# Kernel optimization log

Hardware: AMD Instinct MI355X
Metric: run time of the kernel (lower is better)

## Reference

```python
import jax, jax.numpy as jnp
import numpy as np

D = 3  # input dim, hardcoded in source


def _jet_linear(c0, c1, c2, W, b):
    # Taylor-mode (raw-derivative coefficients) through y = x @ W^T + b.
    # Bias only affects the 0th coefficient; higher coefficients are linear.
    y0 = jnp.einsum('bdi,oi->bdo', c0, W) + b
    y1 = jnp.einsum('bdi,oi->bdo', c1, W)
    y2 = jnp.einsum('bdi,oi->bdo', c2, W)
    return y0, y1, y2


def _jet_tanh(c0, c1, c2):
    # g(t) with g(0)=c0, g'(0)=c1, g''(0)=c2; f = tanh(g):
    #   f(0)  = tanh(c0)
    #   f'(0) = sech^2(c0) * c1
    #   f''(0)= sech^2(c0) * c2 - 2 tanh(c0) sech^2(c0) * c1^2
    y0 = jnp.tanh(c0)
    s = 1.0 - y0 * y0  # sech^2
    y1 = s * c1
    y2 = s * c2 - 2.0 * y0 * s * (c1 * c1)
    return y0, y1, y2


def setup_inputs() -> dict:
    key = jax.random.key(0)
    ks = jax.random.split(key, 7)
    B = 131072
    x = jax.random.normal(ks[0], (B, D), dtype=jnp.float32)
    # Kaiming-ish small init so tanh does not saturate
    W1 = jax.random.normal(ks[1], (128, D), dtype=jnp.float32) * (1.0 / np.sqrt(D))
    b1 = jax.random.normal(ks[2], (128,), dtype=jnp.float32) * 0.01
    W2 = jax.random.normal(ks[3], (64, 128), dtype=jnp.float32) * (1.0 / np.sqrt(128))
    b2 = jax.random.normal(ks[4], (64,), dtype=jnp.float32) * 0.01
    W3 = jax.random.normal(ks[5], (1, 64), dtype=jnp.float32) * (1.0 / np.sqrt(64))
    b3 = jax.random.normal(ks[6], (1,), dtype=jnp.float32) * 0.01
    return {'x': x, 'W1': W1, 'b1': b1, 'W2': W2, 'b2': b2, 'W3': W3, 'b3': b3}


def reference(x, W1, b1, W2, b2, W3, b3):
    # x: [B, D]. Propagate a k=2 jet along each of the D coordinate
    # directions (vmapped over the direction axis d), then sum the 2nd
    # coefficients -> Laplacian. Returns [B, 1].
    B = x.shape[0]
    dt = x.dtype
    X0 = jnp.broadcast_to(x[:, None, :], (B, D, D))            # replicate(x, D)
    X1 = jnp.broadcast_to(jnp.eye(D, dtype=dt), (B, D, D))     # eye(D)
    X2 = jnp.zeros((B, D, D), dtype=dt)                         # zeros(D, D)
    c = _jet_linear(X0, X1, X2, W1, b1)
    c = _jet_tanh(*c)
    c = _jet_linear(*c, W2, b2)
    c = _jet_tanh(*c)
    F0, F1, F2 = _jet_linear(*c, W3, b3)                        # F2: [B, D, 1]
    return F2.sum(axis=1)                                       # sum_vmapped -> [B, 1]
```

## Files before the change

### kernel.cpp

```cpp
#include <hip/hip_runtime.h>


typedef _Float16 h2 __attribute__((ext_vector_type(2)));
typedef _Float16 h4 __attribute__((ext_vector_type(4)));
typedef _Float16 h8 __attribute__((ext_vector_type(8)));
typedef float f32x4 __attribute__((ext_vector_type(4)));

#define BLOCK 256
constexpr int DH1 = 128;
constexpr int DH2 = 64;

constexpr size_t WS_APACK = 0;
constexpr size_t WS_W1P   = 16384;
constexpr size_t WS_WQ2   = 18432;

__device__ __forceinline__ float fast_tanh(float x) {
    float e = __builtin_amdgcn_exp2f(x * 2.885390081777926814f);
    return fmaf(-2.0f, __builtin_amdgcn_rcpf(e + 1.0f), 1.0f);
}

__device__ __forceinline__ h2 pk(float a, float b) {
    auto r = __builtin_amdgcn_cvt_pkrtz(a, b);
    return __builtin_bit_cast(h2, r);
}

__device__ __forceinline__ h8 cat4(h2 a, h2 b, h2 c, h2 d) {
    h4 lo = __builtin_shufflevector(a, b, 0, 1, 2, 3);
    h4 hi = __builtin_shufflevector(c, d, 0, 1, 2, 3);
    return __builtin_shufflevector(lo, hi, 0, 1, 2, 3, 4, 5, 6, 7);
}

__global__ void pack_kernel(const float* __restrict__ W1, const float* __restrict__ b1,
                            const float* __restrict__ W2,
                            _Float16* __restrict__ apack,
                            float4* __restrict__ w1p, float* __restrict__ wq2)
{
    const int t = threadIdx.x, bid = blockIdx.x;
    #pragma unroll
    for (int u = 0; u < 4; ++u) {
        const int e  = bid * 1024 + u * 256 + t;
        const int i  = e & 7;
        const int l  = (e >> 3) & 63;
        const int m  = (e >> 9) & 3;
        const int kk = (e >> 11) & 3;
        const int k  = m * 16 + (l & 15);
        const int j  = kk * 32 + (l >> 4) * 8 + i;
        apack[e] = (_Float16)W2[k * DH1 + j];
    }
    if (bid == 0 && t < DH1) {
        const float wx = W1[t*3+0], wy = W1[t*3+1], wz = W1[t*3+2];
        w1p[t] = make_float4(wx, wy, wz, b1[t]);
        wq2[t] = -2.0f * (wx*wx + wy*wy + wz*wz);
    }
}

__global__ __launch_bounds__(BLOCK, 3) void lap_main(
        const float* __restrict__ x,
        const h8* __restrict__ apack,
        const float4* __restrict__ w1p, const float* __restrict__ wq2,
        const float* __restrict__ b2, const float* __restrict__ w3,
        float* __restrict__ out, int B)
{
    const int t    = threadIdx.x;
    const int lane = t & 63;
    const int wave = t >> 6;
    const int bcol = lane & 15;
    const int g    = lane >> 4;
    const int braw = blockIdx.x * 64 + wave * 16 + bcol;
    const int b    = (braw < B) ? braw : (B - 1);

    const float x0 = x[b*3+0];
    const float x1 = x[b*3+1];
    const float x2 = x[b*3+2];

    f32x4 acc[5][4];
    #pragma unroll
    for (int f = 0; f < 5; ++f)
        #pragma unroll
        for (int m = 0; m < 4; ++m)
            acc[f][m] = (f32x4){0.f, 0.f, 0.f, 0.f};

    #pragma unroll
    for (int kk = 0; kk < 4; ++kk) {
        h8 fa[4];
        #pragma unroll
        for (int m = 0; m < 4; ++m)
            fa[m] = apack[(kk*4 + m) * 64 + lane];

        h2 P0[4], P1[4], P2[4], P3[4], P4[4];
        #pragma unroll
        for (int ii = 0; ii < 4; ++ii) {
            const int j0 = kk*32 + g*8 + ii*2;
            const float4 wa = w1p[j0];
            const float4 wb = w1p[j0 + 1];
            const float  qa = wq2[j0];
            const float  qb = wq2[j0 + 1];

            const float prea = fmaf(x0, wa.x, fmaf(x1, wa.y, fmaf(x2, wa.z, wa.w)));
            const float ea   = __builtin_amdgcn_exp2f(prea * 2.885390081777926814f);
            const float ra   = __builtin_amdgcn_rcpf(ea + 1.0f);
            const float ha   = fmaf(-2.0f, ra, 1.0f);
            const float sa   = fmaf(-ha, ha, 1.0f);

            const float preb = fmaf(x0, wb.x, fmaf(x1, wb.y, fmaf(x2, wb.z, wb.w)));
            const float eb   = __builtin_amdgcn_exp2f(preb * 2.885390081777926814f);
            const float rb   = __builtin_amdgcn_rcpf(eb + 1.0f);
            const float hb   = fmaf(-2.0f, rb, 1.0f);
            const float sb   = fmaf(-hb, hb, 1.0f);

            P0[ii] = pk(ha,          hb);
            P1[ii] = pk(sa * wa.x,   sb * wb.x);
            P2[ii] = pk(sa * wa.y,   sb * wb.y);
            P3[ii] = pk(sa * wa.z,   sb * wb.z);
            P4[ii] = pk((ha*sa)*qa,  (hb*sb)*qb);
        }
        const h8 F0 = cat4(P0[0], P0[1], P0[2], P0[3]);
        const h8 F1 = cat4(P1[0], P1[1], P1[2], P1[3]);
        const h8 F2 = cat4(P2[0], P2[1], P2[2], P2[3]);
        const h8 F3 = cat4(P3[0], P3[1], P3[2], P3[3]);
        const h8 F4 = cat4(P4[0], P4[1], P4[2], P4[3]);

        #pragma unroll
        for (int m = 0; m < 4; ++m) {
            acc[0][m] = __builtin_amdgcn_mfma_f32_16x16x32_f16(fa[m], F0, acc[0][m], 0, 0, 0);
            acc[1][m] = __builtin_amdgcn_mfma_f32_16x16x32_f16(fa[m], F1, acc[1][m], 0, 0, 0);
            acc[2][m] = __builtin_amdgcn_mfma_f32_16x16x32_f16(fa[m], F2, acc[2][m], 0, 0, 0);
            acc[3][m] = __builtin_amdgcn_mfma_f32_16x16x32_f16(fa[m], F3, acc[3][m], 0, 0, 0);
            acc[4][m] = __builtin_amdgcn_mfma_f32_16x16x32_f16(fa[m], F4, acc[4][m], 0, 0, 0);
        }
    }

    float partial = 0.0f;
    #pragma unroll
    for (int m = 0; m < 4; ++m) {
        const int kb = m*16 + g*4;
        const f32x4 b2v = *reinterpret_cast<const f32x4*>(b2 + kb);
        const f32x4 w3v = *reinterpret_cast<const f32x4*>(w3 + kb);
        #pragma unroll
        for (int r = 0; r < 4; ++r) {
            const float z0 = acc[0][m][r] + b2v[r];
            const float g0 = fast_tanh(z0);
            const float s2 = fmaf(-g0, g0, 1.0f);
            const float qd = acc[1][m][r]*acc[1][m][r]
                           + acc[2][m][r]*acc[2][m][r]
                           + acc[3][m][r]*acc[3][m][r];
            const float G2 = s2 * fmaf(-2.0f * g0, qd, acc[4][m][r]);
            partial = fmaf(w3v[r], G2, partial);
        }
    }

    partial += __shfl_xor(partial, 16);
    partial += __shfl_xor(partial, 32);

    if (g == 0 && braw < B) out[braw] = partial;
}

extern "C" void kernel_launch(void* const* d_in, const int* in_sizes, int n_in,
                              void* d_out, int out_size, void* d_ws, size_t ws_size,
                              hipStream_t stream) {
    const float* x  = (const float*)d_in[0];
    const float* W1 = (const float*)d_in[1];
    const float* b1 = (const float*)d_in[2];
    const float* W2 = (const float*)d_in[3];
    const float* b2 = (const float*)d_in[4];
    const float* W3 = (const float*)d_in[5];
    float* out = (float*)d_out;

    char* ws = (char*)d_ws;
    _Float16* apack = (_Float16*)(ws + WS_APACK);
    float4*   w1p   = (float4*)  (ws + WS_W1P);
    float*    wq2   = (float*)   (ws + WS_WQ2);

    const int B = in_sizes[0] / 3;

    pack_kernel<<<8, BLOCK, 0, stream>>>(W1, b1, W2, apack, w1p, wq2);

    const int grid = (B + 63) / 64;
    lap_main<<<grid, BLOCK, 0, stream>>>(x, (const h8*)apack, w1p, wq2, b2, W3, out, B);
}
```

Baseline: 28.25 us.

## Fuse weight packing into main kernel and stage weights in shared memory

Removes the separate pack kernel launch: every block now converts W2 to fp16 in the MFMA fragment layout, precomputes the W1/bias and squared-norm terms, and stages them together with b2 and W3 in LDS before the main computation. Operand loads in the inner loop now come from LDS instead of global memory. Launch bounds rise to 4 blocks per CU. This saves one kernel launch and its dependency, but each of the 2048 blocks redoes the 32KB W2 read, conversion and a barrier, and the higher occupancy target tightens the register budget.

```diff
diff --git a/kernel.cpp b/kernel.cpp
--- a/kernel.cpp
+++ b/kernel.cpp
@@ -9,10 +9,6 @@
 #define BLOCK 256
 constexpr int DH1 = 128;
 constexpr int DH2 = 64;
-
-constexpr size_t WS_APACK = 0;
-constexpr size_t WS_W1P   = 16384;
-constexpr size_t WS_WQ2   = 18432;
 
 __device__ __forceinline__ float fast_tanh(float x) {
     float e = __builtin_amdgcn_exp2f(x * 2.885390081777926814f);
@@ -30,38 +26,44 @@
     return __builtin_shufflevector(lo, hi, 0, 1, 2, 3, 4, 5, 6, 7);
 }
 
-__global__ void pack_kernel(const float* __restrict__ W1, const float* __restrict__ b1,
-                            const float* __restrict__ W2,
-                            _Float16* __restrict__ apack,
-                            float4* __restrict__ w1p, float* __restrict__ wq2)
+__global__ __launch_bounds__(BLOCK, 4) void lap_fused(
+        const float* __restrict__ x,
+        const float* __restrict__ W1, const float* __restrict__ b1,
+        const float* __restrict__ W2, const float* __restrict__ b2,
+        const float* __restrict__ W3,
+        float* __restrict__ out, int B)
 {
-    const int t = threadIdx.x, bid = blockIdx.x;
+    __shared__ float4 s_w1p[DH1];
+    __shared__ float  s_wq2[DH1];
+    __shared__ __align__(16) _Float16 s_a[16][64][8];
+    __shared__ float s_b2[DH2];
+    __shared__ float s_w3[DH2];
+
+    const int t = threadIdx.x;
+
     #pragma unroll
     for (int u = 0; u < 4; ++u) {
-        const int e  = bid * 1024 + u * 256 + t;
-        const int i  = e & 7;
-        const int l  = (e >> 3) & 63;
-        const int m  = (e >> 9) & 3;
-        const int kk = (e >> 11) & 3;
+        const int f  = u * 256 + t;
+        const int l  = f & 63;
+        const int row = f >> 6;
+        const int m  = row & 3;
+        const int kk = row >> 2;
         const int k  = m * 16 + (l & 15);
-        const int j  = kk * 32 + (l >> 4) * 8 + i;
-        apack[e] = (_Float16)W2[k * DH1 + j];
+        const int jr = kk * 32 + (l >> 4) * 8;
+        const float4 wlo = *reinterpret_cast<const float4*>(W2 + k * DH1 + jr);
+        const float4 whi = *reinterpret_cast<const float4*>(W2 + k * DH1 + jr + 4);
+        *reinterpret_cast<h8*>(&s_a[row][l][0]) =
+            cat4(pk(wlo.x, wlo.y), pk(wlo.z, wlo.w),
+                 pk(whi.x, whi.y), pk(whi.z, whi.w));
     }
-    if (bid == 0 && t < DH1) {
+    if (t < DH1) {
         const float wx = W1[t*3+0], wy = W1[t*3+1], wz = W1[t*3+2];
-        w1p[t] = make_float4(wx, wy, wz, b1[t]);
-        wq2[t] = -2.0f * (wx*wx + wy*wy + wz*wz);
+        s_w1p[t] = make_float4(wx, wy, wz, b1[t]);
+        s_wq2[t] = -2.0f * (wx*wx + wy*wy + wz*wz);
     }
-}
+    if (t < DH2) { s_b2[t] = b2[t]; s_w3[t] = W3[t]; }
+    __syncthreads();
 
-__global__ __launch_bounds__(BLOCK, 3) void lap_main(
-        const float* __restrict__ x,
-        const h8* __restrict__ apack,
-        const float4* __restrict__ w1p, const float* __restrict__ wq2,
-        const float* __restrict__ b2, const float* __restrict__ w3,
-        float* __restrict__ out, int B)
-{
-    const int t    = threadIdx.x;
     const int lane = t & 63;
     const int wave = t >> 6;
     const int bcol = lane & 15;
@@ -82,19 +84,14 @@
 
     #pragma unroll
     for (int kk = 0; kk < 4; ++kk) {
-        h8 fa[4];
-        #pragma unroll
-        for (int m = 0; m < 4; ++m)
-            fa[m] = apack[(kk*4 + m) * 64 + lane];
-
         h2 P0[4], P1[4], P2[4], P3[4], P4[4];
         #pragma unroll
         for (int ii = 0; ii < 4; ++ii) {
             const int j0 = kk*32 + g*8 + ii*2;
-            const float4 wa = w1p[j0];
-            const float4 wb = w1p[j0 + 1];
-            const float  qa = wq2[j0];
-            const float  qb = wq2[j0 + 1];
+            const float4 wa = s_w1p[j0];
+            const float4 wb = s_w1p[j0 + 1];
+            const float  qa = s_wq2[j0];
+            const float  qb = s_wq2[j0 + 1];
 
             const float prea = fmaf(x0, wa.x, fmaf(x1, wa.y, fmaf(x2, wa.z, wa.w)));
             const float ea   = __builtin_amdgcn_exp2f(prea * 2.885390081777926814f);
@@ -122,30 +119,29 @@
 
         #pragma unroll
         for (int m = 0; m < 4; ++m) {
-            acc[0][m] = __builtin_amdgcn_mfma_f32_16x16x32_f16(fa[m], F0, acc[0][m], 0, 0, 0);
-            acc[1][m] = __builtin_amdgcn_mfma_f32_16x16x32_f16(fa[m], F1, acc[1][m], 0, 0, 0);
-            acc[2][m] = __builtin_amdgcn_mfma_f32_16x16x32_f16(fa[m], F2, acc[2][m], 0, 0, 0);
-            acc[3][m] = __builtin_amdgcn_mfma_f32_16x16x32_f16(fa[m], F3, acc[3][m], 0, 0, 0);
-            acc[4][m] = __builtin_amdgcn_mfma_f32_16x16x32_f16(fa[m], F4, acc[4][m], 0, 0, 0);
+            const h8 fa = *reinterpret_cast<const h8*>(&s_a[kk*4 + m][lane][0]);
+            acc[0][m] = __builtin_amdgcn_mfma_f32_16x16x32_f16(fa, F0, acc[0][m], 0, 0, 0);
+            acc[1][m] = __builtin_amdgcn_mfma_f32_16x16x32_f16(fa, F1, acc[1][m], 0, 0, 0);
+            acc[2][m] = __builtin_amdgcn_mfma_f32_16x16x32_f16(fa, F2, acc[2][m], 0, 0, 0);
+            acc[3][m] = __builtin_amdgcn_mfma_f32_16x16x32_f16(fa, F3, acc[3][m], 0, 0, 0);
+            acc[4][m] = __builtin_amdgcn_mfma_f32_16x16x32_f16(fa, F4, acc[4][m], 0, 0, 0);
         }
     }
 
     float partial = 0.0f;
     #pragma unroll
     for (int m = 0; m < 4; ++m) {
-        const int kb = m*16 + g*4;
-        const f32x4 b2v = *reinterpret_cast<const f32x4*>(b2 + kb);
-        const f32x4 w3v = *reinterpret_cast<const f32x4*>(w3 + kb);
         #pragma unroll
         for (int r = 0; r < 4; ++r) {
-            const float z0 = acc[0][m][r] + b2v[r];
+            const int k = m*16 + g*4 + r;
+            const float z0 = acc[0][m][r] + s_b2[k];
             const float g0 = fast_tanh(z0);
             const float s2 = fmaf(-g0, g0, 1.0f);
             const float qd = acc[1][m][r]*acc[1][m][r]
                            + acc[2][m][r]*acc[2][m][r]
                            + acc[3][m][r]*acc[3][m][r];
             const float G2 = s2 * fmaf(-2.0f * g0, qd, acc[4][m][r]);
-            partial = fmaf(w3v[r], G2, partial);
+            partial = fmaf(s_w3[k], G2, partial);
         }
     }
 
@@ -166,15 +162,7 @@
     const float* W3 = (const float*)d_in[5];
     float* out = (float*)d_out;
 
-    char* ws = (char*)d_ws;
-    _Float16* apack = (_Float16*)(ws + WS_APACK);
-    float4*   w1p   = (float4*)  (ws + WS_W1P);
-    float*    wq2   = (float*)   (ws + WS_WQ2);
-
     const int B = in_sizes[0] / 3;
-
-    pack_kernel<<<8, BLOCK, 0, stream>>>(W1, b1, W2, apack, w1p, wq2);
-
     const int grid = (B + 63) / 64;
-    lap_main<<<grid, BLOCK, 0, stream>>>(x, (const h8*)apack, w1p, wq2, b2, W3, out, B);
+    lap_fused<<<grid, BLOCK, 0, stream>>>(x, W1, b1, W2, b2, W3, out, B);
 }
```

Measured after the change: 31.95 us. 1.13x slower.
